# Optimization experiments

Hardware: AMD Instinct MI355X
Metric: run time of the kernel (lower is better)

Reference implementation:

```python
import jax, jax.numpy as jnp
import numpy as np

H, KVH, HD = 32, 8, 128          # query heads, kv heads, head_dim
HIDDEN = H * HD                   # 4096
TOTAL_KV = 3072                   # sum of (start_pos + seqlen) over the batch (static)
ROPE_THETA = 10000.0


def setup_inputs() -> dict:
    key = jax.random.key(0)
    ks = jax.random.split(key, 4)
    x = jax.random.normal(ks[0], (1024, HIDDEN), jnp.float32)
    wqkv = jax.random.normal(ks[1], (HIDDEN, HIDDEN + 2 * KVH * HD), jnp.float32) * 0.02
    wo = jax.random.normal(ks[2], (HIDDEN, HIDDEN), jnp.float32) * 0.02
    # paged cache: [num_layers=1, 2(k/v), cache_slots, kv_heads, head_dim], holds post-RoPE prefixes
    kv_cache = jax.random.normal(ks[3], (1, 2, 8192, KVH, HD), jnp.float32) * 0.02
    # 4 ragged requests: seqlens [512,256,128,128], cached prefixes [0,512,1024,512]
    seqstarts = jnp.array([0, 512, 768, 896, 1024], jnp.int32)
    start_pos = jnp.array([0, 512, 1024, 512], jnp.int32)
    kvstarts = jnp.array([0, 512, 1280, 2432, 3072], jnp.int32)  # cumsum of start_pos+seqlen
    cachestarts = jnp.array([0, 1024, 2560, 4096], jnp.int32)    # page base per request
    return dict(x=x, wqkv=wqkv, wo=wo, kv_cache=kv_cache, seqstarts=seqstarts,
                kvstarts=kvstarts, cachestarts=cachestarts, start_pos=start_pos)


def _rope(t, pos):
    # interleaved (GPT-J style) rotary over full head_dim; t: [T, nheads, HD], pos: [T]
    d2 = HD // 2
    inv_freq = 1.0 / (ROPE_THETA ** (jnp.arange(d2, dtype=jnp.float32) / d2))
    ang = pos.astype(jnp.float32)[:, None] * inv_freq      # [T, d2]
    cos = jnp.cos(ang)[:, None, :]
    sin = jnp.sin(ang)[:, None, :]
    x1, x2 = t[..., 0::2], t[..., 1::2]
    r1 = x1 * cos - x2 * sin
    r2 = x1 * sin + x2 * cos
    return jnp.stack([r1, r2], axis=-1).reshape(t.shape)


def _forward(x, wqkv, wo, kv_cache, seqstarts, kvstarts, cachestarts, start_pos):
    T = x.shape[0]
    # fused QKV projection
    xqkv = (x @ wqkv).reshape(T, H + 2 * KVH, HD)
    xq, xk, xv = jnp.split(xqkv, [H, H + KVH], axis=1)   # [T,32,HD],[T,8,HD],[T,8,HD]

    # per-token batch id and absolute position (ragged via seqstarts)
    tok = jnp.arange(T)
    bq = jnp.searchsorted(seqstarts, tok, side='right') - 1
    pos_q = tok - seqstarts[bq] + start_pos[bq]
    xq = _rope(xq, pos_q)
    xk = _rope(xk, pos_q)

    # assemble ragged KV stream: cached prefix (paged cache) + freshly projected tokens
    kvtok = jnp.arange(TOTAL_KV)
    bkv = jnp.searchsorted(kvstarts, kvtok, side='right') - 1
    pkv = kvtok - kvstarts[bkv]                              # absolute kv position
    is_new = pkv >= start_pos[bkv]
    new_idx = jnp.clip(seqstarts[bkv] + pkv - start_pos[bkv], 0, T - 1)
    cache_idx = cachestarts[bkv] + pkv                       # paged slot for prefix
    keys = jnp.where(is_new[:, None, None], xk[new_idx], kv_cache[0, 0][cache_idx])
    vals = jnp.where(is_new[:, None, None], xv[new_idx], kv_cache[0, 1][cache_idx])

    # GQA: repeat kv heads to match query heads
    rep = H // KVH
    keys = jnp.repeat(keys, rep, axis=1)                     # [TOTAL_KV, 32, HD]
    vals = jnp.repeat(vals, rep, axis=1)

    scale = 1.0 / jnp.sqrt(jnp.float32(HD))
    scores = jnp.einsum('qhd,khd->hqk', xq, keys) * scale    # [32, T, TOTAL_KV]
    # ragged causal mask: same request and kv position <= query position
    mask = (bq[:, None] == bkv[None, :]) & (pkv[None, :] <= pos_q[:, None])
    scores = jnp.where(mask[None], scores, jnp.float32(-1e30))
    probs = jax.nn.softmax(scores, axis=-1)
    attn = jnp.einsum('hqk,khd->qhd', probs, vals)           # [T, 32, HD]
    return attn.reshape(T, HIDDEN) @ wo


def reference(x, wqkv, wo, kv_cache, seqstarts, kvstarts, cachestarts, start_pos):
    return _forward(x, wqkv, wo, kv_cache, seqstarts, kvstarts, cachestarts, start_pos)
```

## Files before the change

### kernel.cpp

```cpp
#include <hip/hip_runtime.h>
#include <hip/hip_bf16.h>
#include <math.h>
#include <stdint.h>

typedef __bf16 bf16;
typedef __attribute__((ext_vector_type(4))) float floatx4;
typedef __attribute__((ext_vector_type(8))) bf16 bf16x8;
typedef __attribute__((ext_vector_type(4))) bf16 bf16x4;

#define LDS_ASYNC16(gptr, lptr)                                                \
  __builtin_amdgcn_global_load_lds(                                            \
      (const __attribute__((address_space(1))) void*)(gptr),                   \
      (__attribute__((address_space(3))) void*)(lptr), 16, 0, 0)

__global__ __launch_bounds__(256) void k_cvt(const float* __restrict__ in,
                                             bf16* __restrict__ out) {
  int i = (blockIdx.x * 256 + threadIdx.x) * 4;
  float4 v = *(const float4*)(in + i);
  bf16x4 o;
  o[0] = (bf16)v.x; o[1] = (bf16)v.y; o[2] = (bf16)v.z; o[3] = (bf16)v.w;
  *(bf16x4*)(out + i) = o;
}

__global__ __launch_bounds__(256) void k_merge(const float* __restrict__ a,
                                               const float* __restrict__ b,
                                               float* __restrict__ out) {
  int i = (blockIdx.x * 256 + threadIdx.x) * 4;
  float4 va = *(const float4*)(a + i);
  float4 vb = *(const float4*)(b + i);
  float4 o;
  o.x = va.x + vb.x; o.y = va.y + vb.y; o.z = va.z + vb.z; o.w = va.w + vb.w;
  *(float4*)(out + i) = o;
}

__global__ __launch_bounds__(256) void k_transpose_cvt(const float* __restrict__ in,
                                                       bf16* __restrict__ out,
                                                       int K, int N) {
  __shared__ float tile[64][65];
  int k0 = blockIdx.y * 64, n0 = blockIdx.x * 64;
  int tid = threadIdx.x;
  int cg = tid & 15, rr = tid >> 4;
#pragma unroll
  for (int p = 0; p < 4; ++p) {
    int r = rr + p * 16;
    float4 v = *(const float4*)(in + (size_t)(k0 + r) * N + n0 + cg * 4);
    tile[r][cg * 4 + 0] = v.x; tile[r][cg * 4 + 1] = v.y;
    tile[r][cg * 4 + 2] = v.z; tile[r][cg * 4 + 3] = v.w;
  }
  __syncthreads();
#pragma unroll
  for (int p = 0; p < 4; ++p) {
    int n = rr + p * 16;
    bf16x4 o;
    o[0] = (bf16)tile[cg * 4 + 0][n];
    o[1] = (bf16)tile[cg * 4 + 1][n];
    o[2] = (bf16)tile[cg * 4 + 2][n];
    o[3] = (bf16)tile[cg * 4 + 3][n];
    *(bf16x4*)(out + (size_t)(n0 + n) * K + k0 + cg * 4) = o;
  }
}

__global__ __launch_bounds__(256) void k_gemm_bt(const bf16* __restrict__ A,
                                                 const bf16* __restrict__ B,
                                                 float* __restrict__ C,
                                                 int M, int N, int K, int ksplit) {
  __shared__ bf16 As[128 * 32];
  __shared__ bf16 Bs[128 * 32];
  int tid = threadIdx.x;
  int w = tid >> 6, lane = tid & 63;
  int lq = lane >> 4, l16 = lane & 15;
  int bm = blockIdx.y * 128, bn = blockIdx.x * 128;
  int wm = (w >> 1) * 64, wn = (w & 1) * 64;
  int kc = K / ksplit;
  int koff = blockIdx.z * kc;
  C += (size_t)blockIdx.z * M * N;
  floatx4 acc[4][4] = {};
  const bf16* Ab = A + (size_t)bm * K;
  const bf16* Bb = B + (size_t)bn * K;
  int srow = (lane >> 2);
  int scol = (((lane & 3) ^ ((srow >> 1) & 3))) * 8;
  int sa = (l16 >> 1) & 3;

  for (int k0 = koff; k0 < koff + kc; k0 += 32) {
#pragma unroll
    for (int c = 0; c < 2; ++c) {
      int r = w * 32 + c * 16 + srow;
      LDS_ASYNC16(Ab + (size_t)r * K + k0 + scol, &As[(w * 32 + c * 16) * 32]);
      LDS_ASYNC16(Bb + (size_t)r * K + k0 + scol, &Bs[(w * 32 + c * 16) * 32]);
    }
    __syncthreads();
    bf16x8 af[4], bfr[4];
#pragma unroll
    for (int i = 0; i < 4; ++i)
      af[i] = *(const bf16x8*)&As[(wm + i * 16 + l16) * 32 + (lq ^ sa) * 8];
#pragma unroll
    for (int j = 0; j < 4; ++j)
      bfr[j] = *(const bf16x8*)&Bs[(wn + j * 16 + l16) * 32 + (lq ^ sa) * 8];
#pragma unroll
    for (int i = 0; i < 4; ++i)
#pragma unroll
      for (int j = 0; j < 4; ++j)
        acc[i][j] = __builtin_amdgcn_mfma_f32_16x16x32_bf16(af[i], bfr[j],
                                                            acc[i][j], 0, 0, 0);
    __syncthreads();
  }
#pragma unroll
  for (int i = 0; i < 4; ++i)
#pragma unroll
    for (int j = 0; j < 4; ++j) {
      int m = bm + wm + i * 16 + lq * 4;
      int n = bn + wn + j * 16 + l16;
      float* cp = C + (size_t)m * N + n;
#pragma unroll
      for (int r = 0; r < 4; ++r) cp[(size_t)r * N] = acc[i][j][r];
    }
}

__global__ __launch_bounds__(256) void k_rope(const float* __restrict__ xp0,
                                              const float* __restrict__ xp1,
                                              bf16* __restrict__ qb,
                                              bf16* __restrict__ kb,
                                              const int* __restrict__ seqstarts,
                                              const int* __restrict__ start_pos) {
  int t = blockIdx.x;
  int s = 0;
  for (int i = 1; i < 4; ++i) if (seqstarts[i] <= t) s = i;
  float pos = (float)(t - seqstarts[s] + start_pos[s]);
  for (int wk = threadIdx.x; wk < 40 * 64; wk += 256) {
    int hh = wk >> 6, j = wk & 63;
    size_t idx = ((size_t)t * 48 + hh) * 128 + 2 * j;
    float2 a0 = *(const float2*)(xp0 + idx);
    float2 a1 = *(const float2*)(xp1 + idx);
    float x1 = a0.x + a1.x;
    float x2 = a0.y + a1.y;
    float invf = exp2f(-(float)j * 0.20762050593045935f);
    float ang = pos * invf;
    float sv, cv;
    sincosf(ang, &sv, &cv);
    float r1 = x1 * cv - x2 * sv;
    float r2 = x1 * sv + x2 * cv;
    unsigned int u1 = (unsigned int)__builtin_bit_cast(unsigned short, (bf16)r1);
    unsigned int u2 = (unsigned int)__builtin_bit_cast(unsigned short, (bf16)r2);
    unsigned int pk = u1 | (u2 << 16);
    unsigned int* dst = (hh < 32)
        ? (unsigned int*)(qb + ((size_t)t * 32 + hh) * 128)
        : (unsigned int*)(kb + ((size_t)t * 8 + (hh - 32)) * 128);
    dst[j] = pk;
  }
}

__global__ __launch_bounds__(256) void k_assemble_k(
    const bf16* __restrict__ xk, const float* __restrict__ ck,
    bf16* __restrict__ kall,
    const int* __restrict__ seqstarts, const int* __restrict__ kvstarts,
    const int* __restrict__ cachestarts, const int* __restrict__ start_pos) {
  int p = blockIdx.x;
  int b = 0;
  for (int i = 1; i < 4; ++i) if (kvstarts[i] <= p) b = i;
  int pkv = p - kvstarts[b];
  int tid = threadIdx.x;
  int hk = tid >> 5, d4 = (tid & 31) * 4;
  bf16* dst = kall + ((size_t)hk * 3072 + p) * 128 + d4;
  if (pkv >= start_pos[b]) {
    int tn = seqstarts[b] + pkv - start_pos[b];
    *(bf16x4*)dst = *(const bf16x4*)(xk + ((size_t)tn * 8 + hk) * 128 + d4);
  } else {
    int ci = cachestarts[b] + pkv;
    float4 v = *(const float4*)(ck + ((size_t)ci * 8 + hk) * 128 + d4);
    bf16x4 o;
    o[0] = (bf16)v.x; o[1] = (bf16)v.y; o[2] = (bf16)v.z; o[3] = (bf16)v.w;
    *(bf16x4*)dst = o;
  }
}

__global__ __launch_bounds__(256) void k_assemble_vT(
    const float* __restrict__ xp0, const float* __restrict__ xp1,
    const float* __restrict__ cv, bf16* __restrict__ vT,
    const int* __restrict__ seqstarts, const int* __restrict__ kvstarts,
    const int* __restrict__ cachestarts, const int* __restrict__ start_pos) {
  __shared__ float tile[64][130];
  int hk = blockIdx.y, p0 = blockIdx.x * 64;
  int tid = threadIdx.x;
  {
    int r = tid >> 2;
    int p = p0 + r;
    int b = 0;
    for (int i = 1; i < 4; ++i) if (kvstarts[i] <= p) b = i;
    int pkv = p - kvstarts[b];
    int f0 = (tid & 3) * 32;
    if (pkv >= start_pos[b]) {
      int tn = seqstarts[b] + pkv - start_pos[b];
      size_t base = (size_t)tn * 6144 + (40 + hk) * 128;
#pragma unroll
      for (int i = 0; i < 8; ++i) {
        float4 v0 = *(const float4*)(xp0 + base + f0 + i * 4);
        float4 v1 = *(const float4*)(xp1 + base + f0 + i * 4);
        tile[r][f0 + i * 4 + 0] = v0.x + v1.x;
        tile[r][f0 + i * 4 + 1] = v0.y + v1.y;
        tile[r][f0 + i * 4 + 2] = v0.z + v1.z;
        tile[r][f0 + i * 4 + 3] = v0.w + v1.w;
      }
    } else {
      int ci = cachestarts[b] + pkv;
      const float* src = cv + ((size_t)ci * 8 + hk) * 128;
#pragma unroll
      for (int i = 0; i < 8; ++i) {
        float4 v = *(const float4*)(src + f0 + i * 4);
        tile[r][f0 + i * 4 + 0] = v.x; tile[r][f0 + i * 4 + 1] = v.y;
        tile[r][f0 + i * 4 + 2] = v.z; tile[r][f0 + i * 4 + 3] = v.w;
      }
    }
  }
  __syncthreads();
  int d = tid >> 1, hf = tid & 1;
  bf16* dst = vT + ((size_t)hk * 128 + d) * 3072 + p0 + hf * 32;
#pragma unroll
  for (int q = 0; q < 4; ++q) {
    bf16x8 o;
#pragma unroll
    for (int e = 0; e < 8; ++e) o[e] = (bf16)tile[hf * 32 + q * 8 + e][d];
    *(bf16x8*)(dst + q * 8) = o;
  }
}

__global__ __launch_bounds__(256) void k_attn(
    const bf16* __restrict__ qb, const bf16* __restrict__ kall,
    const bf16* __restrict__ vT, float* __restrict__ pO,
    float2* __restrict__ pml,
    const int* __restrict__ seqstarts, const int* __restrict__ kvstarts,
    const int* __restrict__ start_pos) {
  __shared__ bf16 Ks[64 * 128];
  __shared__ bf16 Vs[128 * 64];
  __shared__ bf16 Ps[64 * 64];
  int qbi = blockIdx.x, h = blockIdx.y, seg = blockIdx.z, hk = h >> 2;
  int t0 = qbi * 64;
  int s = 0;
  for (int i = 1; i < 4; ++i) if (seqstarts[i] <= t0) s = i;
  int posbase = t0 - seqstarts[s] + start_pos[s];
  int kv0 = kvstarts[s];
  int nkv = posbase + 64;
  int pbeg = seg * 512;
  if (pbeg >= nkv) return;
  int pend = min(pbeg + 512, nkv);
  int tid = threadIdx.x, w = tid >> 6, lane = tid & 63;
  int lq = lane >> 4, l16 = lane & 15;

  bf16x8 qa[4];
#pragma unroll
  for (int kk = 0; kk < 4; ++kk)
    qa[kk] = *(const bf16x8*)(qb + (((size_t)(t0 + w * 16 + l16) * 32 + h) * 128 +
                                    kk * 32 + lq * 8));

  int krow = lane >> 4;
  int vrow = lane >> 3;
  int vchunk = ((lane & 7) ^ (vrow & 7));
  int sw8 = l16 & 7;

  float m_r[4], l_r[4];
  floatx4 oacc[8] = {};
#pragma unroll
  for (int rg = 0; rg < 4; ++rg) { m_r[rg] = -3.0e38f; l_r[rg] = 0.f; }
  const float scale = 0.08838834764831845f;

  for (int p0 = pbeg; p0 < pend; p0 += 64) {
#pragma unroll
    for (int c = 0; c < 4; ++c) {
      int base_r = w * 16 + c * 4;
      int r = base_r + krow;
      int gch = (lane & 15) ^ ((c * 4 + krow) & 15);
      LDS_ASYNC16(kall + (((size_t)hk * 3072 + kv0 + p0 + r) * 128 + gch * 8),
                  &Ks[base_r * 128]);
    }
#pragma unroll
    for (int c = 0; c < 4; ++c) {
      int base_d = w * 32 + c * 8;
      int d = base_d + vrow;
      LDS_ASYNC16(vT + (((size_t)hk * 128 + d) * 3072 + kv0 + p0 + vchunk * 8),
                  &Vs[base_d * 64]);
    }
    __syncthreads();

    floatx4 sacc[4] = {};
#pragma unroll
    for (int kk = 0; kk < 4; ++kk)
#pragma unroll
      for (int j = 0; j < 4; ++j) {
        bf16x8 kb = *(const bf16x8*)&Ks[(j * 16 + l16) * 128 +
                                        ((kk * 4 + lq) ^ l16) * 8];
        sacc[j] = __builtin_amdgcn_mfma_f32_16x16x32_bf16(qa[kk], kb, sacc[j], 0, 0, 0);
      }

#pragma unroll
    for (int rg = 0; rg < 4; ++rg) {
      int qpos = posbase + w * 16 + lq * 4 + rg;
      float sv[4];
      float rmax = -3.0e38f;
#pragma unroll
      for (int j = 0; j < 4; ++j) {
        int pkv = p0 + j * 16 + l16;
        sv[j] = (pkv <= qpos) ? sacc[j][rg] * scale : -3.0e38f;
        rmax = fmaxf(rmax, sv[j]);
      }
#pragma unroll
      for (int off = 1; off < 16; off <<= 1)
        rmax = fmaxf(rmax, __shfl_xor(rmax, off, 64));
      float mnew = fmaxf(m_r[rg], rmax);
      float alpha = __expf(m_r[rg] - mnew);
      m_r[rg] = mnew;
      int prow = w * 16 + lq * 4 + rg;
      int pswz = (lq * 4 + rg) & 7;
      float psum = 0.f;
#pragma unroll
      for (int j = 0; j < 4; ++j) {
        float pv = __expf(sv[j] - mnew);
        psum += pv;
        int chunk = (j * 2 + (l16 >> 3)) ^ pswz;
        Ps[prow * 64 + chunk * 8 + (l16 & 7)] = (bf16)pv;
      }
#pragma unroll
      for (int off = 1; off < 16; off <<= 1) psum += __shfl_xor(psum, off, 64);
      l_r[rg] = l_r[rg] * alpha + psum;
#pragma unroll
      for (int nt = 0; nt < 8; ++nt) oacc[nt][rg] *= alpha;
    }

#pragma unroll
    for (int kk = 0; kk < 2; ++kk) {
      bf16x8 pa = *(const bf16x8*)&Ps[(w * 16 + l16) * 64 +
                                      ((kk * 4 + lq) ^ sw8) * 8];
#pragma unroll
      for (int nt = 0; nt < 8; ++nt) {
        bf16x8 vb = *(const bf16x8*)&Vs[(nt * 16 + l16) * 64 +
                                        ((kk * 4 + lq) ^ sw8) * 8];
        oacc[nt] = __builtin_amdgcn_mfma_f32_16x16x32_bf16(pa, vb, oacc[nt], 0, 0, 0);
      }
    }
    __syncthreads();
  }

  size_t obase = (((size_t)seg * 16 + qbi) * 32 + h) * 8192;
#pragma unroll
  for (int rg = 0; rg < 4; ++rg) {
    int row = w * 16 + lq * 4 + rg;
#pragma unroll
    for (int nt = 0; nt < 8; ++nt)
      pO[obase + (size_t)row * 128 + nt * 16 + l16] = oacc[nt][rg];
    if (l16 == 0)
      pml[(((size_t)seg * 16 + qbi) * 32 + h) * 64 + row] =
          make_float2(m_r[rg], l_r[rg]);
  }
}

__global__ __launch_bounds__(256) void k_attn_merge(
    const float* __restrict__ pO, const float2* __restrict__ pml,
    bf16* __restrict__ aout,
    const int* __restrict__ seqstarts, const int* __restrict__ start_pos) {
  int qbi = blockIdx.x, h = blockIdx.y;
  int t0 = qbi * 64;
  int s = 0;
  for (int i = 1; i < 4; ++i) if (seqstarts[i] <= t0) s = i;
  int nkv = t0 - seqstarts[s] + start_pos[s] + 64;
  int ns = (nkv + 511) >> 9;
  int tid = threadIdx.x;
  int row = tid >> 2, cg = (tid & 3) * 32;
  float2 ml[3];
  float w[3];
  float mstar = -3.0e38f;
  for (int si = 0; si < ns; ++si) {
    ml[si] = pml[(((size_t)si * 16 + qbi) * 32 + h) * 64 + row];
    mstar = fmaxf(mstar, ml[si].x);
  }
  float denom = 0.f;
  for (int si = 0; si < ns; ++si) {
    w[si] = __expf(ml[si].x - mstar);
    denom += w[si] * ml[si].y;
  }
  float inv = 1.0f / denom;
  bf16* dst = aout + (size_t)(t0 + row) * 4096 + h * 128 + cg;
#pragma unroll
  for (int c = 0; c < 32; c += 8) {
    float acc[8] = {};
    for (int si = 0; si < ns; ++si) {
      const float* src = pO + (((size_t)si * 16 + qbi) * 32 + h) * 8192 +
                         (size_t)row * 128 + cg + c;
      float4 v0 = *(const float4*)(src);
      float4 v1 = *(const float4*)(src + 4);
      acc[0] += w[si] * v0.x; acc[1] += w[si] * v0.y;
      acc[2] += w[si] * v0.z; acc[3] += w[si] * v0.w;
      acc[4] += w[si] * v1.x; acc[5] += w[si] * v1.y;
      acc[6] += w[si] * v1.z; acc[7] += w[si] * v1.w;
    }
    bf16x8 o;
#pragma unroll
    for (int e = 0; e < 8; ++e) o[e] = (bf16)(acc[e] * inv);
    *(bf16x8*)(dst + c) = o;
  }
}

extern "C" void kernel_launch(void* const* d_in, const int* in_sizes, int n_in,
                              void* d_out, int out_size, void* d_ws, size_t ws_size,
                              hipStream_t stream) {
  const float* x = (const float*)d_in[0];
  const float* wqkv = (const float*)d_in[1];
  const float* wo = (const float*)d_in[2];
  const float* kv = (const float*)d_in[3];
  const int* seqstarts = (const int*)d_in[4];
  const int* kvstarts = (const int*)d_in[5];
  const int* cachestarts = (const int*)d_in[6];
  const int* start_pos = (const int*)d_in[7];
  float* out = (float*)d_out;

  char* base = (char*)d_ws;
  size_t off = 0;
  auto carve = [&](size_t bytes) {
    void* r = base + off;
    off += (bytes + 255) & ~(size_t)255;
    return r;
  };
  bf16* x_bf    = (bf16*)carve(1024ull * 4096 * 2);
  bf16* wqkvT   = (bf16*)carve(6144ull * 4096 * 2);
  bf16* woT     = (bf16*)carve(4096ull * 4096 * 2);
  float* xqkv   = (float*)carve(2ull * 1024 * 6144 * 4);
  bf16* q_bf    = (bf16*)carve(1024ull * 32 * 128 * 2);
  bf16* xk_bf   = (bf16*)carve(1024ull * 8 * 128 * 2);
  bf16* k_all   = (bf16*)carve(8ull * 3072 * 128 * 2);
  bf16* vT_all  = (bf16*)carve(8ull * 128 * 3072 * 2);
  bf16* attn_bf = (bf16*)carve(1024ull * 4096 * 2);
  float2* pml   = (float2*)carve(3ull * 16 * 32 * 64 * 8);
  float* outp = (float*)wqkvT;
  float* pO = xqkv;

  float* xqkv1 = xqkv + 1024ull * 6144;
  const float* cache_v = kv + 8192ull * 8 * 128;

  k_cvt<<<4096, 256, 0, stream>>>(x, x_bf);
  k_transpose_cvt<<<dim3(96, 64), 256, 0, stream>>>(wqkv, wqkvT, 4096, 6144);
  k_transpose_cvt<<<dim3(64, 64), 256, 0, stream>>>(wo, woT, 4096, 4096);
  k_gemm_bt<<<dim3(48, 8, 2), 256, 0, stream>>>(x_bf, wqkvT, xqkv, 1024, 6144,
                                                4096, 2);
  k_rope<<<1024, 256, 0, stream>>>(xqkv, xqkv1, q_bf, xk_bf, seqstarts, start_pos);
  k_assemble_k<<<3072, 256, 0, stream>>>(xk_bf, kv, k_all, seqstarts, kvstarts,
                                         cachestarts, start_pos);
  k_assemble_vT<<<dim3(48, 8), 256, 0, stream>>>(xqkv, xqkv1, cache_v, vT_all,
                                                 seqstarts, kvstarts, cachestarts,
                                                 start_pos);
  k_attn<<<dim3(16, 32, 3), 256, 0, stream>>>(q_bf, k_all, vT_all, pO, pml,
                                              seqstarts, kvstarts, start_pos);
  k_attn_merge<<<dim3(16, 32), 256, 0, stream>>>(pO, pml, attn_bf, seqstarts,
                                                 start_pos);
  k_gemm_bt<<<dim3(32, 8, 2), 256, 0, stream>>>(attn_bf, woT, outp, 1024, 4096,
                                                4096, 2);
  k_merge<<<4096, 256, 0, stream>>>(outp, outp + 1024ull * 4096, out);
}
```

Before: 495.3 us.

## Replace GEMM with triple-buffered 128x256 tile kernel and drop QKV split-K

```diff
diff --git a/kernel.cpp b/kernel.cpp
--- a/kernel.cpp
+++ b/kernel.cpp
@@ -60,64 +60,110 @@
   }
 }
 
-__global__ __launch_bounds__(256) void k_gemm_bt(const bf16* __restrict__ A,
-                                                 const bf16* __restrict__ B,
-                                                 float* __restrict__ C,
-                                                 int M, int N, int K, int ksplit) {
-  __shared__ bf16 As[128 * 32];
-  __shared__ bf16 Bs[128 * 32];
+__global__ __launch_bounds__(512) void k_gemm8(const bf16* __restrict__ A,
+                                               const bf16* __restrict__ B,
+                                               float* __restrict__ C,
+                                               int M, int N, int K, int ksplit) {
+  __shared__ bf16 As[3][128 * 64];
+  __shared__ bf16 Bs[3][256 * 64];
   int tid = threadIdx.x;
   int w = tid >> 6, lane = tid & 63;
   int lq = lane >> 4, l16 = lane & 15;
-  int bm = blockIdx.y * 128, bn = blockIdx.x * 128;
-  int wm = (w >> 1) * 64, wn = (w & 1) * 64;
+  int wr = w >> 2, wc = w & 3;
+  int bm = blockIdx.y * 128, bn = blockIdx.x * 256;
   int kc = K / ksplit;
-  int koff = blockIdx.z * kc;
+  int NT = kc >> 6;
   C += (size_t)blockIdx.z * M * N;
+  const bf16* Ab = A + (size_t)bm * K + blockIdx.z * kc;
+  const bf16* Bb = B + (size_t)bn * K + blockIdx.z * kc;
+  int srow = w * 8 + (lane >> 3);
+  int sx = ((lane & 7) ^ (srow & 7)) * 8;
+  const bf16* Asrc = Ab + (size_t)srow * K + sx;
+  const bf16* Bsrc = Bb + (size_t)srow * K + sx;
+  bf16* AL = &As[0][0] + w * 8 * 64;
+  bf16* BL = &Bs[0][0] + w * 8 * 64;
+
+#define STAGE8(bi, t)                                                          \
+  do {                                                                         \
+    const bf16* a_ = Asrc + (size_t)(t) * 64;                                  \
+    const bf16* b_ = Bsrc + (size_t)(t) * 64;                                  \
+    LDS_ASYNC16(a_, AL + (bi) * (128 * 64));                                   \
+    LDS_ASYNC16(a_ + (size_t)64 * K, AL + (bi) * (128 * 64) + 64 * 64);        \
+    LDS_ASYNC16(b_, BL + (bi) * (256 * 64));                                   \
+    LDS_ASYNC16(b_ + (size_t)64 * K, BL + (bi) * (256 * 64) + 64 * 64);        \
+    LDS_ASYNC16(b_ + (size_t)128 * K, BL + (bi) * (256 * 64) + 128 * 64);      \
+    LDS_ASYNC16(b_ + (size_t)192 * K, BL + (bi) * (256 * 64) + 192 * 64);      \
+  } while (0)
+
+  STAGE8(0, 0);
+  STAGE8(1, 1);
+
+  int aoff[4][2], boff[4][2];
+#pragma unroll
+  for (int i = 0; i < 4; ++i)
+#pragma unroll
+    for (int kk = 0; kk < 2; ++kk) {
+      int sw = ((kk * 4 + lq) ^ (l16 & 7)) * 8;
+      aoff[i][kk] = (wr * 64 + i * 16 + l16) * 64 + sw;
+      boff[i][kk] = (wc * 64 + i * 16 + l16) * 64 + sw;
+    }
+
   floatx4 acc[4][4] = {};
-  const bf16* Ab = A + (size_t)bm * K;
-  const bf16* Bb = B + (size_t)bn * K;
-  int srow = (lane >> 2);
-  int scol = (((lane & 3) ^ ((srow >> 1) & 3))) * 8;
-  int sa = (l16 >> 1) & 3;
-
-  for (int k0 = koff; k0 < koff + kc; k0 += 32) {
-#pragma unroll
-    for (int c = 0; c < 2; ++c) {
-      int r = w * 32 + c * 16 + srow;
-      LDS_ASYNC16(Ab + (size_t)r * K + k0 + scol, &As[(w * 32 + c * 16) * 32]);
-      LDS_ASYNC16(Bb + (size_t)r * K + k0 + scol, &Bs[(w * 32 + c * 16) * 32]);
-    }
-    __syncthreads();
-    bf16x8 af[4], bfr[4];
+
+  auto compute_tile = [&](int bcc) {
+    const bf16* Ar = &As[bcc][0];
+    const bf16* Br = &Bs[bcc][0];
+    bf16x8 af[4][2], bg[4][2];
 #pragma unroll
     for (int i = 0; i < 4; ++i)
-      af[i] = *(const bf16x8*)&As[(wm + i * 16 + l16) * 32 + (lq ^ sa) * 8];
-#pragma unroll
-    for (int j = 0; j < 4; ++j)
-      bfr[j] = *(const bf16x8*)&Bs[(wn + j * 16 + l16) * 32 + (lq ^ sa) * 8];
+#pragma unroll
+      for (int kk = 0; kk < 2; ++kk) {
+        af[i][kk] = *(const bf16x8*)(Ar + aoff[i][kk]);
+        bg[i][kk] = *(const bf16x8*)(Br + boff[i][kk]);
+      }
+    __builtin_amdgcn_s_setprio(1);
 #pragma unroll
     for (int i = 0; i < 4; ++i)
 #pragma unroll
       for (int j = 0; j < 4; ++j)
-        acc[i][j] = __builtin_amdgcn_mfma_f32_16x16x32_bf16(af[i], bfr[j],
-                                                            acc[i][j], 0, 0, 0);
-    __syncthreads();
-  }
+#pragma unroll
+        for (int kk = 0; kk < 2; ++kk)
+          acc[i][j] = __builtin_amdgcn_mfma_f32_16x16x32_bf16(af[i][kk], bg[j][kk],
+                                                              acc[i][j], 0, 0, 0);
+    __builtin_amdgcn_s_setprio(0);
+  };
+
+  int bc = 0;
+  for (int t = 0; t < NT - 1; ++t) {
+    asm volatile("s_waitcnt vmcnt(6)" ::: "memory");
+    __builtin_amdgcn_s_barrier();
+    __builtin_amdgcn_sched_barrier(0);
+    if (t + 2 < NT) {
+      int bs = bc + 2; if (bs >= 3) bs -= 3;
+      STAGE8(bs, t + 2);
+    }
+    compute_tile(bc);
+    ++bc; if (bc == 3) bc = 0;
+  }
+  asm volatile("s_waitcnt vmcnt(0)" ::: "memory");
+  __builtin_amdgcn_s_barrier();
+  __builtin_amdgcn_sched_barrier(0);
+  compute_tile(bc);
+#undef STAGE8
+
 #pragma unroll
   for (int i = 0; i < 4; ++i)
 #pragma unroll
     for (int j = 0; j < 4; ++j) {
-      int m = bm + wm + i * 16 + lq * 4;
-      int n = bn + wn + j * 16 + l16;
+      int m = bm + wr * 64 + i * 16 + lq * 4;
+      int n = bn + wc * 64 + j * 16 + l16;
       float* cp = C + (size_t)m * N + n;
 #pragma unroll
       for (int r = 0; r < 4; ++r) cp[(size_t)r * N] = acc[i][j][r];
     }
 }
 
-__global__ __launch_bounds__(256) void k_rope(const float* __restrict__ xp0,
-                                              const float* __restrict__ xp1,
+__global__ __launch_bounds__(256) void k_rope(const float* __restrict__ xp,
                                               bf16* __restrict__ qb,
                                               bf16* __restrict__ kb,
                                               const int* __restrict__ seqstarts,
@@ -129,10 +175,9 @@
   for (int wk = threadIdx.x; wk < 40 * 64; wk += 256) {
     int hh = wk >> 6, j = wk & 63;
     size_t idx = ((size_t)t * 48 + hh) * 128 + 2 * j;
-    float2 a0 = *(const float2*)(xp0 + idx);
-    float2 a1 = *(const float2*)(xp1 + idx);
-    float x1 = a0.x + a1.x;
-    float x2 = a0.y + a1.y;
+    float2 a0 = *(const float2*)(xp + idx);
+    float x1 = a0.x;
+    float x2 = a0.y;
     float invf = exp2f(-(float)j * 0.20762050593045935f);
     float ang = pos * invf;
     float sv, cv;
@@ -174,7 +219,7 @@
 }
 
 __global__ __launch_bounds__(256) void k_assemble_vT(
-    const float* __restrict__ xp0, const float* __restrict__ xp1,
+    const float* __restrict__ xp,
     const float* __restrict__ cv, bf16* __restrict__ vT,
     const int* __restrict__ seqstarts, const int* __restrict__ kvstarts,
     const int* __restrict__ cachestarts, const int* __restrict__ start_pos) {
@@ -193,12 +238,11 @@
       size_t base = (size_t)tn * 6144 + (40 + hk) * 128;
 #pragma unroll
       for (int i = 0; i < 8; ++i) {
-        float4 v0 = *(const float4*)(xp0 + base + f0 + i * 4);
-        float4 v1 = *(const float4*)(xp1 + base + f0 + i * 4);
-        tile[r][f0 + i * 4 + 0] = v0.x + v1.x;
-        tile[r][f0 + i * 4 + 1] = v0.y + v1.y;
-        tile[r][f0 + i * 4 + 2] = v0.z + v1.z;
-        tile[r][f0 + i * 4 + 3] = v0.w + v1.w;
+        float4 v0 = *(const float4*)(xp + base + f0 + i * 4);
+        tile[r][f0 + i * 4 + 0] = v0.x;
+        tile[r][f0 + i * 4 + 1] = v0.y;
+        tile[r][f0 + i * 4 + 2] = v0.z;
+        tile[r][f0 + i * 4 + 3] = v0.w;
       }
     } else {
       int ci = cachestarts[b] + pkv;
@@ -430,25 +474,24 @@
   float* outp = (float*)wqkvT;
   float* pO = xqkv;
 
-  float* xqkv1 = xqkv + 1024ull * 6144;
   const float* cache_v = kv + 8192ull * 8 * 128;
 
   k_cvt<<<4096, 256, 0, stream>>>(x, x_bf);
   k_transpose_cvt<<<dim3(96, 64), 256, 0, stream>>>(wqkv, wqkvT, 4096, 6144);
   k_transpose_cvt<<<dim3(64, 64), 256, 0, stream>>>(wo, woT, 4096, 4096);
-  k_gemm_bt<<<dim3(48, 8, 2), 256, 0, stream>>>(x_bf, wqkvT, xqkv, 1024, 6144,
-                                                4096, 2);
-  k_rope<<<1024, 256, 0, stream>>>(xqkv, xqkv1, q_bf, xk_bf, seqstarts, start_pos);
+  k_gemm8<<<dim3(24, 8, 1), 512, 0, stream>>>(x_bf, wqkvT, xqkv, 1024, 6144,
+                                              4096, 1);
+  k_rope<<<1024, 256, 0, stream>>>(xqkv, q_bf, xk_bf, seqstarts, start_pos);
   k_assemble_k<<<3072, 256, 0, stream>>>(xk_bf, kv, k_all, seqstarts, kvstarts,
                                          cachestarts, start_pos);
-  k_assemble_vT<<<dim3(48, 8), 256, 0, stream>>>(xqkv, xqkv1, cache_v, vT_all,
+  k_assemble_vT<<<dim3(48, 8), 256, 0, stream>>>(xqkv, cache_v, vT_all,
                                                  seqstarts, kvstarts, cachestarts,
                                                  start_pos);
   k_attn<<<dim3(16, 32, 3), 256, 0, stream>>>(q_bf, k_all, vT_all, pO, pml,
                                               seqstarts, kvstarts, start_pos);
   k_attn_merge<<<dim3(16, 32), 256, 0, stream>>>(pO, pml, attn_bf, seqstarts,
                                                  start_pos);
-  k_gemm_bt<<<dim3(32, 8, 2), 256, 0, stream>>>(attn_bf, woT, outp, 1024, 4096,
-                                                4096, 2);
+  k_gemm8<<<dim3(16, 8, 2), 512, 0, stream>>>(attn_bf, woT, outp, 1024, 4096,
+                                              4096, 2);
   k_merge<<<4096, 256, 0, stream>>>(outp, outp + 1024ull * 4096, out);
 }
```

New measurement: 488.4 us. No clear change (-1.4%).
